# Optimization experiments

Measured on AMD Instinct MI355X. Metric: run time of the kernel, lower is better.

Reference implementation:

```python
import jax, jax.numpy as jnp
import numpy as np

N, L, V, D, E, NL = 50000, 32, 5000, 128, 800000, 3
P, B = 5000, 64

def setup_inputs() -> dict:
    key = jax.random.key(0)
    ks = jax.random.split(key, 6)
    x = jax.random.randint(ks[0], (N, L), 0, V)            # token ids, 0 = pad
    edge_index = jax.random.randint(ks[1], (2, E), 0, N)   # [2,E] src,dst
    pool_idx = jnp.arange(N) // (N // P)                   # node -> pooled supernode
    node_batch = pool_idx * B // P                         # node -> graph id (grouped, as in torch loop)
    embed = jax.random.normal(ks[2], (V, D), jnp.float32) * 0.02
    W_l = jax.random.normal(ks[3], (NL, D, D), jnp.float32) / np.sqrt(D)
    W_r = jax.random.normal(ks[4], (NL, D, D), jnp.float32) / np.sqrt(D)
    b = jnp.zeros((NL, D), jnp.float32)
    return dict(x=x, edge_index=edge_index, pool_idx=pool_idx, node_batch=node_batch,
                num_pooled=P, embed=embed, W_l=W_l, W_r=W_r, b=b)

def reference(x, edge_index, pool_idx, node_batch, num_pooled, embed, W_l, W_r, b):
    n = x.shape[0]
    dt = embed.dtype
    # masked mean-pool of token embeddings (pad id = 0), length clamped to >=1
    mask = (x != 0)
    lengths = jnp.clip(mask.sum(axis=1), 1, None).astype(dt)          # [N]
    h = (embed[x] * mask[..., None].astype(dt)).sum(axis=1) / lengths[:, None]  # [N,D]
    src, dst = edge_index[0], edge_index[1]
    deg = jnp.clip(jax.ops.segment_sum(jnp.ones(src.shape[0], dt), dst, num_segments=n), 1.0, None)
    # SAGEConv layers: mean-aggregate neighbors, lin_l(agg)+bias + lin_r(self), relu
    # (dropout p=0.5 is identity in eval mode)
    for i in range(W_l.shape[0]):
        agg = jax.ops.segment_sum(h[src], dst, num_segments=n) / deg[:, None]
        h = jax.nn.relu(agg @ W_l[i] + b[i] + h @ W_r[i])
    # global mean pool over supernodes
    cnt = jnp.clip(jax.ops.segment_sum(jnp.ones(n, dt), pool_idx, num_segments=num_pooled), 1.0, None)
    x_pooled = jax.ops.segment_sum(h, pool_idx, num_segments=num_pooled) / cnt[:, None]
    # global max pool of graph ids -> pooled batch vector
    batch_pooled = jax.ops.segment_max(node_batch, pool_idx, num_segments=num_pooled)
    # coalesced pooled edges without self-loops, as a dense boolean adjacency
    sp, dp = pool_idx[src], pool_idx[dst]
    adj = jnp.zeros((num_pooled, num_pooled), jnp.bool_).at[sp, dp].set(True)
    adj = adj & ~jnp.eye(num_pooled, dtype=jnp.bool_)
    return x_pooled, adj, batch_pooled
```

## Files before the change

kernel.cpp:

```cpp
#include <hip/hip_runtime.h>
#include <hip/hip_fp16.h>
#include <limits.h>

#define D 128
#define NBK 768
#define EB  2048
#define SCL 64.0f

typedef __attribute__((ext_vector_type(8))) short bf16x8;
typedef __attribute__((ext_vector_type(4))) float f32x4;
typedef __attribute__((ext_vector_type(2))) float f32x2;

#if __has_builtin(__builtin_amdgcn_cvt_pk_f32_fp8) && __has_builtin(__builtin_amdgcn_cvt_pk_fp8_f32)
#define HW_FP8 1
#endif

static __device__ __forceinline__ unsigned short f2bf(float f) {
    unsigned u = __builtin_bit_cast(unsigned, f);
    u += 0x7FFFu + ((u >> 16) & 1u);
    return (unsigned short)(u >> 16);
}
static __device__ __forceinline__ float bf2f(unsigned u16) {
    unsigned u = u16 << 16;
    return __builtin_bit_cast(float, u);
}
static __device__ __forceinline__ bf16x8 load_frag(const unsigned short* p) {
    uint4 v = *(const uint4*)p;
    return __builtin_bit_cast(bf16x8, v);
}
static __device__ __forceinline__ ushort4 pack4(const float* a, float s) {
    ushort4 o;
    o.x = f2bf(a[0] * s); o.y = f2bf(a[1] * s);
    o.z = f2bf(a[2] * s); o.w = f2bf(a[3] * s);
    return o;
}

static __device__ __forceinline__ unsigned char f2q(float v) {
#ifdef HW_FP8
    return (unsigned char)(__builtin_amdgcn_cvt_pk_fp8_f32(v, v, 0, false) & 0xff);
#else
    unsigned short u = __half_as_ushort(__float2half(v));
    u = (unsigned short)(u + 0x7F + ((u >> 8) & 1));
    return (unsigned char)(u >> 8);
#endif
}
static __device__ __forceinline__ unsigned enc4(float a0, float a1, float a2, float a3) {
#ifdef HW_FP8
    unsigned u = __builtin_amdgcn_cvt_pk_fp8_f32(a0, a1, 0, false);
    u = __builtin_amdgcn_cvt_pk_fp8_f32(a2, a3, (int)u, true);
    return u;
#else
    return (unsigned)f2q(a0) | ((unsigned)f2q(a1) << 8) |
           ((unsigned)f2q(a2) << 16) | ((unsigned)f2q(a3) << 24);
#endif
}
static __device__ __forceinline__ void dec4(float* a, unsigned u) {
#ifdef HW_FP8
    f32x2 lo = __builtin_amdgcn_cvt_pk_f32_fp8((int)u, false);
    f32x2 hi = __builtin_amdgcn_cvt_pk_f32_fp8((int)u, true);
    a[0] += lo.x; a[1] += lo.y; a[2] += hi.x; a[3] += hi.y;
#else
    a[0] += __half2float(__ushort_as_half((unsigned short)((u & 0xff) << 8)));
    a[1] += __half2float(__ushort_as_half((unsigned short)(((u >> 8) & 0xff) << 8)));
    a[2] += __half2float(__ushort_as_half((unsigned short)(((u >> 16) & 0xff) << 8)));
    a[3] += __half2float(__ushort_as_half((unsigned short)((u >> 24) << 8)));
#endif
}
static __device__ __forceinline__ void dec16(float* a, uint4 v) {
    dec4(a, v.x); dec4(a + 4, v.y); dec4(a + 8, v.z); dec4(a + 12, v.w);
}

__global__ __launch_bounds__(256) void zero_k(float4* __restrict__ b, size_t nb)
{
    size_t i = (size_t)blockIdx.x * 256 + threadIdx.x;
    if (i < nb) b[i] = make_float4(0.f, 0.f, 0.f, 0.f);
}

__global__ __launch_bounds__(256) void epack_k(
    const float* __restrict__ embed, unsigned* __restrict__ e8, int n4)
{
    int i = blockIdx.x * 256 + threadIdx.x;
    if (i >= n4) return;
    float4 v = *(const float4*)&embed[(size_t)i * 4];
    e8[i] = enc4(v.x * SCL, v.y * SCL, v.z * SCL, v.w * SCL);
}

__global__ __launch_bounds__(256) void embed_pool_k(
    const int* __restrict__ x, const unsigned char* __restrict__ e8,
    unsigned short* __restrict__ h16, unsigned char* __restrict__ h8, int n, int L)
{
    __shared__ int toks[16][32];
    int t = threadIdx.x;
    int sub = t >> 4, s = t & 15;
    int node = blockIdx.x * 16 + sub;
    for (int j = t; j < 16 * L; j += 256) {
        int nd = blockIdx.x * 16 + j / L;
        toks[j / L][j % L] = (nd < n) ? x[(size_t)nd * L + (j % L)] : 0;
    }
    __syncthreads();
    if (node >= n) return;
    float acc[8] = {};
    int cnt = 0;
    for (int l = 0; l < L; ++l) {
        int tok = toks[sub][l];
        if (tok != 0) {
            uint2 v = *(const uint2*)&e8[(size_t)tok * D + s * 8];
            dec4(acc, v.x); dec4(acc + 4, v.y);
            cnt++;
        }
    }
    float c = (float)(cnt > 0 ? cnt : 1);
    float invh = 1.0f / (SCL * c);
    float inv8 = 1.0f / c;
    ushort4 lo = pack4(acc, invh), hi = pack4(acc + 4, invh);
    *(ushort4*)&h16[(size_t)node * D + s * 8]     = lo;
    *(ushort4*)&h16[(size_t)node * D + s * 8 + 4] = hi;
    uint2 q;
    q.x = enc4(acc[0] * inv8, acc[1] * inv8, acc[2] * inv8, acc[3] * inv8);
    q.y = enc4(acc[4] * inv8, acc[5] * inv8, acc[6] * inv8, acc[7] * inv8);
    *(uint2*)&h8[(size_t)node * D + s * 8] = q;
}

__global__ __launch_bounds__(256) void wpack_k(
    const float* __restrict__ Wl, const float* __restrict__ Wr,
    unsigned short* __restrict__ Wp, int NL)
{
    int idx = blockIdx.x * 256 + threadIdx.x;
    if (idx >= NL * 2 * 16384) return;
    int m = idx >> 14;
    int r = idx & 16383;
    int j = r & 7;
    int lane = (r >> 3) & 63;
    int cb = (r >> 9) & 7;
    int kb = (r >> 12) & 3;
    const float* W = ((m & 1) ? Wr : Wl) + (size_t)(m >> 1) * D * D;
    int k = kb * 32 + (lane >> 4) * 8 + j;
    int c = cb * 16 + (lane & 15);
    Wp[idx] = f2bf(W[(size_t)k * D + c]);
}

__global__ __launch_bounds__(256) void deghist_k(
    const int* __restrict__ ei, const int* __restrict__ pool,
    int* __restrict__ degall, int E, int n, int P, int nblk)
{
    __shared__ int hist[NBK];
    int t = threadIdx.x;
    for (int i = t; i < NBK; i += 256) hist[i] = 0;
    __syncthreads();
    int base = blockIdx.x * EB;
    int lim = min(E, base + EB);
    for (int e = base + t; e < lim; e += 256) {
        int src = ei[e], dst = ei[E + e];
        atomicAdd(&degall[dst], 1);
        int sp = pool[src], dp = pool[dst];
        if (sp != dp) atomicAdd(&hist[(sp * P + dp) >> 15], 1);
    }
    __syncthreads();
    for (int i = t; i < NBK; i += 256)
        degall[n + i * nblk + blockIdx.x] = hist[i];
}

__global__ __launch_bounds__(256) void scan_partial_k(
    const int* __restrict__ deg, int* __restrict__ bsum, int n)
{
    int b = blockIdx.x, t = threadIdx.x;
    int i0 = b * 1024 + t * 4;
    int s = 0;
    #pragma unroll
    for (int k = 0; k < 4; ++k) { int i = i0 + k; if (i < n) s += deg[i]; }
    for (int off = 32; off > 0; off >>= 1) s += __shfl_down(s, off, 64);
    __shared__ int sm4[4];
    if ((t & 63) == 0) sm4[t >> 6] = s;
    __syncthreads();
    if (t == 0) bsum[b] = sm4[0] + sm4[1] + sm4[2] + sm4[3];
}

__global__ __launch_bounds__(512) void scan_bsum_k(
    const int* __restrict__ bsum, int* __restrict__ boff, int nb)
{
    __shared__ int sm[512];
    int t = threadIdx.x;
    sm[t] = (t < nb) ? bsum[t] : 0;
    __syncthreads();
    for (int off = 1; off < 512; off <<= 1) {
        int add = (t >= off) ? sm[t - off] : 0;
        __syncthreads();
        sm[t] += add;
        __syncthreads();
    }
    if (t < nb) boff[t] = (t > 0) ? sm[t - 1] : 0;
}

__global__ __launch_bounds__(256) void scan_final_k(
    const int* __restrict__ deg, const int* __restrict__ boff,
    int* __restrict__ rp, int n)
{
    __shared__ int sm[256];
    int b = blockIdx.x, t = threadIdx.x;
    int i0 = b * 1024 + t * 4;
    int v[4];
    #pragma unroll
    for (int k = 0; k < 4; ++k) { int i = i0 + k; v[k] = (i < n) ? deg[i] : 0; }
    v[1] += v[0]; v[2] += v[1]; v[3] += v[2];
    sm[t] = v[3];
    __syncthreads();
    for (int off = 1; off < 256; off <<= 1) {
        int add = (t >= off) ? sm[t - off] : 0;
        __syncthreads();
        sm[t] += add;
        __syncthreads();
    }
    int base = boff[b] + ((t > 0) ? sm[t - 1] : 0);
    if (b == 0 && t == 0) rp[0] = 0;
    #pragma unroll
    for (int k = 0; k < 4; ++k) {
        int i = i0 + k;
        if (i < n) rp[i + 1] = base + v[k];
    }
}

__global__ __launch_bounds__(256) void csr_scatter_k(
    const int* __restrict__ ei, const int* __restrict__ rpall,
    int* __restrict__ cur, int* __restrict__ col, int E)
{
    int e = blockIdx.x * 256 + threadIdx.x;
    if (e >= E) return;
    int src = ei[e], dst = ei[E + e];
    int pos = atomicAdd(&cur[dst], 1);
    col[rpall[dst] + pos] = src;
}

__global__ __launch_bounds__(256) void bkt_scatter_k(
    const int* __restrict__ ei, const int* __restrict__ rpall,
    const int* __restrict__ pool, int* __restrict__ kbuf,
    int E, int n, int P, int nblk)
{
    __shared__ int off[NBK];
    int t = threadIdx.x;
    for (int i = t; i < NBK; i += 256)
        off[i] = rpall[n + i * nblk + blockIdx.x] - E;
    __syncthreads();
    int base = blockIdx.x * EB;
    int lim = min(E, base + EB);
    for (int e = base + t; e < lim; e += 256) {
        int src = ei[e], dst = ei[E + e];
        int sp = pool[src], dp = pool[dst];
        if (sp != dp) {
            int key = sp * P + dp;
            int kpos = atomicAdd(&off[key >> 15], 1);
            kbuf[kpos] = key;
        }
    }
}

__global__ __launch_bounds__(256) void adj_write_k(
    const int* __restrict__ rpall, const int* __restrict__ kbuf,
    float* __restrict__ adj, int E, int n, int nblk, int ns)
{
    int b = blockIdx.x;
    int s = rpall[n + b * nblk] - E;
    int e = (b == NBK - 1) ? (rpall[ns] - E) : (rpall[n + (b + 1) * nblk] - E);
    for (int i = s + threadIdx.x; i < e; i += 256)
        adj[(size_t)kbuf[i]] = 1.0f;
}

__global__ __launch_bounds__(256) void aggregate_k(
    const unsigned char* __restrict__ h8, const int* __restrict__ rp,
    const int* __restrict__ col, unsigned short* __restrict__ agg16, int n)
{
    int node = blockIdx.x * 4 + (threadIdx.x >> 6);
    int lane = threadIdx.x & 63;
    if (node >= n) return;
    int beg = rp[node], end = rp[node + 1];
    int oct = lane >> 3, s = lane & 7;
    float acc[16] = {};
    int e = beg + oct;
    for (; e + 8 < end; e += 16) {
        uint4 v0 = *(const uint4*)&h8[(size_t)col[e] * D + s * 16];
        uint4 v1 = *(const uint4*)&h8[(size_t)col[e + 8] * D + s * 16];
        dec16(acc, v0);
        dec16(acc, v1);
    }
    if (e < end)
        dec16(acc, *(const uint4*)&h8[(size_t)col[e] * D + s * 16]);
    #pragma unroll
    for (int k = 0; k < 16; ++k) {
        acc[k] += __shfl_xor(acc[k], 8, 64);
        acc[k] += __shfl_xor(acc[k], 16, 64);
        acc[k] += __shfl_xor(acc[k], 32, 64);
    }
    if (oct == 0) {
        int dg = end - beg;
        float inv = 1.0f / (SCL * (float)(dg > 0 ? dg : 1));
        ushort4 o0 = pack4(acc, inv),     o1 = pack4(acc + 4, inv);
        ushort4 o2 = pack4(acc + 8, inv), o3 = pack4(acc + 12, inv);
        *(ushort4*)&agg16[(size_t)node * D + s * 16]      = o0;
        *(ushort4*)&agg16[(size_t)node * D + s * 16 + 4]  = o1;
        *(ushort4*)&agg16[(size_t)node * D + s * 16 + 8]  = o2;
        *(ushort4*)&agg16[(size_t)node * D + s * 16 + 12] = o3;
    }
}

__global__ __launch_bounds__(256) void sage_gemm_mfma_k(
    const unsigned short* __restrict__ agg16, unsigned short* __restrict__ h16,
    unsigned char* __restrict__ h8, const unsigned short* __restrict__ Wp,
    const float* __restrict__ bias, int n, int write8)
{
    int t = threadIdx.x;
    int w = t >> 6, lane = t & 63;
    int node0 = blockIdx.x * 128 + w * 32;
    int row = lane & 15, g = lane >> 4;

    f32x4 acc[2][8];
    #pragma unroll
    for (int i = 0; i < 2; ++i)
        #pragma unroll
        for (int c = 0; c < 8; ++c)
            acc[i][c] = (f32x4){0.f, 0.f, 0.f, 0.f};

    float bs[8];
    #pragma unroll
    for (int cb = 0; cb < 8; ++cb) bs[cb] = bias[cb * 16 + row];

    bool ok0 = (node0 < n);
    bool ok1 = (node0 + 16 < n);

    #pragma unroll
    for (int kb = 0; kb < 8; ++kb) {
        const unsigned short* Asrc = (kb < 4) ? agg16 : h16;
        int ko = (kb & 3) * 32 + g * 8;
        bf16x8 a0 = (bf16x8){0,0,0,0,0,0,0,0};
        bf16x8 a1 = a0;
        if (ok0) a0 = load_frag(&Asrc[(size_t)(node0 + row) * D + ko]);
        if (ok1) a1 = load_frag(&Asrc[(size_t)(node0 + 16 + row) * D + ko]);
        const unsigned short* wp = Wp + ((kb < 4) ? 0 : 16384) + (size_t)(kb & 3) * 4096;
        #pragma unroll
        for (int cb = 0; cb < 8; ++cb) {
            bf16x8 b = load_frag(&wp[(cb * 64 + lane) * 8]);
            acc[0][cb] = __builtin_amdgcn_mfma_f32_16x16x32_bf16(a0, b, acc[0][cb], 0, 0, 0);
            acc[1][cb] = __builtin_amdgcn_mfma_f32_16x16x32_bf16(a1, b, acc[1][cb], 0, 0, 0);
        }
    }

    #pragma unroll
    for (int rg = 0; rg < 2; ++rg) {
        int nb = node0 + rg * 16;
        if (nb >= n) break;
        #pragma unroll
        for (int cb = 0; cb < 8; ++cb) {
            int c = cb * 16 + row;
            #pragma unroll
            for (int j = 0; j < 4; ++j) {
                int node = nb + g * 4 + j;
                float v = fmaxf(acc[rg][cb][j] + bs[cb], 0.f);
                h16[(size_t)node * D + c] = f2bf(v);
                if (write8) h8[(size_t)node * D + c] = f2q(v * SCL);
            }
        }
    }
}

__global__ __launch_bounds__(128) void poolmean_k(
    const unsigned short* __restrict__ h16, const int* __restrict__ pool,
    const int* __restrict__ nbatch, float* __restrict__ outx,
    float* __restrict__ outb, int n, int P)
{
    int p = blockIdx.x;
    int d = threadIdx.x;
    int lo = 0, hi = n;
    while (lo < hi) { int mid = (lo + hi) >> 1; if (pool[mid] < p) lo = mid + 1; else hi = mid; }
    int s = lo;
    hi = n;
    while (lo < hi) { int mid = (lo + hi) >> 1; if (pool[mid] < p + 1) lo = mid + 1; else hi = mid; }
    int e = lo;
    float sum = 0.f;
    for (int i = s; i < e; ++i) sum += bf2f(h16[(size_t)i * D + d]);
    int c = e - s;
    outx[(size_t)p * D + d] = sum / (float)(c > 0 ? c : 1);
    if (d == 0) {
        int bm = INT_MIN;
        for (int i = s; i < e; ++i) bm = max(bm, nbatch[i]);
        outb[p] = (float)bm;
    }
}

extern "C" void kernel_launch(void* const* d_in, const int* in_sizes, int n_in,
                              void* d_out, int out_size, void* d_ws, size_t ws_size,
                              hipStream_t stream)
{
    const int*   x      = (const int*)d_in[0];
    const int*   ei     = (const int*)d_in[1];
    const int*   pool   = (const int*)d_in[2];
    const int*   nbatch = (const int*)d_in[3];
    const float* embed  = (const float*)d_in[5];
    const float* Wl     = (const float*)d_in[6];
    const float* Wr     = (const float*)d_in[7];
    const float* bias   = (const float*)d_in[8];

    const int N  = in_sizes[2];
    const int L  = in_sizes[0] / N;
    const int E  = in_sizes[1] / 2;
    const int VD = in_sizes[5];
    const int NL = in_sizes[6] / (D * D);
    const int P  = 5000;

    float* out_x   = (float*)d_out;
    float* out_adj = out_x + (size_t)P * D;
    float* out_b   = out_adj + (size_t)P * P;

    char* w = (char*)d_ws;
    auto alloc = [&](size_t bytes) { void* p = w; w += (bytes + 255) & ~255ULL; return p; };
    size_t ND = (size_t)N * D;
    unsigned short* h16   = (unsigned short*)alloc(ND * 2);
    unsigned short* agg16 = (unsigned short*)alloc(ND * 2);
    unsigned char*  h8    = (unsigned char*)alloc(ND);
    unsigned short* Wp    = (unsigned short*)alloc((size_t)NL * 2 * 16384 * 2);
    unsigned char*  e8    = (unsigned char*)alloc((size_t)VD);

    const int NBLK = (E + EB - 1) / EB;
    const int NS   = N + NBK * NBLK;
    const int NB   = (NS + 1023) / 1024;

    int*   col    = (int*)alloc((size_t)E * 4);
    int*   kbuf   = (int*)alloc((size_t)E * 4);
    int*   rpall  = (int*)alloc((size_t)(NS + 1) * 4);
    int*   bsum   = (int*)alloc(512 * 4);
    int*   boff   = (int*)alloc(512 * 4);
    int*   degall = (int*)alloc((size_t)(NS + N) * 4);
    int*   cur    = degall + NS;

    size_t nz = ((size_t)(NS + N) + 3) / 4;
    zero_k<<<(int)((nz + 255) / 256), 256, 0, stream>>>((float4*)degall, nz);

    epack_k<<<(VD / 4 + 255) / 256, 256, 0, stream>>>(embed, (unsigned*)e8, VD / 4);
    wpack_k<<<(NL * 2 * 16384 + 255) / 256, 256, 0, stream>>>(Wl, Wr, Wp, NL);
    embed_pool_k<<<(N + 15) / 16, 256, 0, stream>>>(x, e8, h16, h8, N, L);
    deghist_k<<<NBLK, 256, 0, stream>>>(ei, pool, degall, E, N, P, NBLK);
    scan_partial_k<<<NB, 256, 0, stream>>>(degall, bsum, NS);
    scan_bsum_k<<<1, 512, 0, stream>>>(bsum, boff, NB);
    scan_final_k<<<NB, 256, 0, stream>>>(degall, boff, rpall, NS);
    csr_scatter_k<<<(E + 255) / 256, 256, 0, stream>>>(ei, rpall, cur, col, E);
    bkt_scatter_k<<<NBLK, 256, 0, stream>>>(ei, rpall, pool, kbuf, E, N, P, NBLK);
    adj_write_k<<<NBK, 256, 0, stream>>>(rpall, kbuf, out_adj, E, N, NBLK, NS);

    for (int ly = 0; ly < NL; ++ly) {
        aggregate_k<<<(N + 3) / 4, 256, 0, stream>>>(h8, rpall, col, agg16, N);
        sage_gemm_mfma_k<<<(N + 127) / 128, 256, 0, stream>>>(
            agg16, h16, h8, Wp + (size_t)ly * 2 * 16384, bias + (size_t)ly * D, N,
            (ly < NL - 1) ? 1 : 0);
    }

    poolmean_k<<<P, 128, 0, stream>>>(h16, pool, nbatch, out_x, out_b, N, P);
}
```

Baseline: 308.9 us.

## Replace bucketed adjacency scatter with atomic bitmap and dense expand

The pooled adjacency is now built by setting bits in a P*P bitmap with atomicOr, then one kernel expands every bitmap word into 32 float writes covering the whole dense output. This drops the per-block histogram, the extended scan over the bucket counts, the key scatter and the sparse adjacency write, so the scan now covers only node degrees. The trade is that every element of the 25M-float adjacency is written by the expand kernel, and the bitmap is zeroed in the same launch as the degree arrays. The aggregate kernel is also reworked to use 16 lanes with 8-byte loads per edge (4 edges in flight instead of 8), and the pool-mean loop is unrolled into four accumulators.

```diff
diff --git a/kernel.cpp b/kernel.cpp
--- a/kernel.cpp
+++ b/kernel.cpp
@@ -3,8 +3,6 @@
 #include <limits.h>
 
 #define D 128
-#define NBK 768
-#define EB  2048
 #define SCL 64.0f
 
 typedef __attribute__((ext_vector_type(8))) short bf16x8;
@@ -66,14 +64,14 @@
     a[3] += __half2float(__ushort_as_half((unsigned short)((u >> 24) << 8)));
 #endif
 }
-static __device__ __forceinline__ void dec16(float* a, uint4 v) {
-    dec4(a, v.x); dec4(a + 4, v.y); dec4(a + 8, v.z); dec4(a + 12, v.w);
-}
-
-__global__ __launch_bounds__(256) void zero_k(float4* __restrict__ b, size_t nb)
+
+__global__ __launch_bounds__(256) void zero_k(
+    float4* __restrict__ a, size_t na, float4* __restrict__ b, size_t nb)
 {
     size_t i = (size_t)blockIdx.x * 256 + threadIdx.x;
-    if (i < nb) b[i] = make_float4(0.f, 0.f, 0.f, 0.f);
+    float4 z = make_float4(0.f, 0.f, 0.f, 0.f);
+    if (i < na) a[i] = z;
+    else if (i - na < nb) b[i - na] = z;
 }
 
 __global__ __launch_bounds__(256) void epack_k(
@@ -83,42 +81,6 @@
     if (i >= n4) return;
     float4 v = *(const float4*)&embed[(size_t)i * 4];
     e8[i] = enc4(v.x * SCL, v.y * SCL, v.z * SCL, v.w * SCL);
-}
-
-__global__ __launch_bounds__(256) void embed_pool_k(
-    const int* __restrict__ x, const unsigned char* __restrict__ e8,
-    unsigned short* __restrict__ h16, unsigned char* __restrict__ h8, int n, int L)
-{
-    __shared__ int toks[16][32];
-    int t = threadIdx.x;
-    int sub = t >> 4, s = t & 15;
-    int node = blockIdx.x * 16 + sub;
-    for (int j = t; j < 16 * L; j += 256) {
-        int nd = blockIdx.x * 16 + j / L;
-        toks[j / L][j % L] = (nd < n) ? x[(size_t)nd * L + (j % L)] : 0;
-    }
-    __syncthreads();
-    if (node >= n) return;
-    float acc[8] = {};
-    int cnt = 0;
-    for (int l = 0; l < L; ++l) {
-        int tok = toks[sub][l];
-        if (tok != 0) {
-            uint2 v = *(const uint2*)&e8[(size_t)tok * D + s * 8];
-            dec4(acc, v.x); dec4(acc + 4, v.y);
-            cnt++;
-        }
-    }
-    float c = (float)(cnt > 0 ? cnt : 1);
-    float invh = 1.0f / (SCL * c);
-    float inv8 = 1.0f / c;
-    ushort4 lo = pack4(acc, invh), hi = pack4(acc + 4, invh);
-    *(ushort4*)&h16[(size_t)node * D + s * 8]     = lo;
-    *(ushort4*)&h16[(size_t)node * D + s * 8 + 4] = hi;
-    uint2 q;
-    q.x = enc4(acc[0] * inv8, acc[1] * inv8, acc[2] * inv8, acc[3] * inv8);
-    q.y = enc4(acc[4] * inv8, acc[5] * inv8, acc[6] * inv8, acc[7] * inv8);
-    *(uint2*)&h8[(size_t)node * D + s * 8] = q;
 }
 
 __global__ __launch_bounds__(256) void wpack_k(
@@ -139,25 +101,55 @@
     Wp[idx] = f2bf(W[(size_t)k * D + c]);
 }
 
-__global__ __launch_bounds__(256) void deghist_k(
+__global__ __launch_bounds__(256) void embed_pool_k(
+    const int* __restrict__ x, const unsigned char* __restrict__ e8,
+    unsigned short* __restrict__ h16, unsigned char* __restrict__ h8, int n, int L)
+{
+    __shared__ int toks[16][32];
+    int t = threadIdx.x;
+    int sub = t >> 4, s = t & 15;
+    int node = blockIdx.x * 16 + sub;
+    for (int j = t; j < 16 * L; j += 256) {
+        int nd = blockIdx.x * 16 + j / L;
+        toks[j / L][j % L] = (nd < n) ? x[(size_t)nd * L + (j % L)] : 0;
+    }
+    __syncthreads();
+    if (node >= n) return;
+    float acc[8] = {};
+    int cnt = 0;
+    for (int l = 0; l < L; ++l) {
+        int tok = toks[sub][l];
+        if (tok != 0) {
+            uint2 v = *(const uint2*)&e8[(size_t)tok * D + s * 8];
+            dec4(acc, v.x); dec4(acc + 4, v.y);
+            cnt++;
+        }
+    }
+    float c = (float)(cnt > 0 ? cnt : 1);
+    float invh = 1.0f / (SCL * c);
+    float inv8 = 1.0f / c;
+    ushort4 lo = pack4(acc, invh), hi = pack4(acc + 4, invh);
+    *(ushort4*)&h16[(size_t)node * D + s * 8]     = lo;
+    *(ushort4*)&h16[(size_t)node * D + s * 8 + 4] = hi;
+    uint2 q;
+    q.x = enc4(acc[0] * inv8, acc[1] * inv8, acc[2] * inv8, acc[3] * inv8);
+    q.y = enc4(acc[4] * inv8, acc[5] * inv8, acc[6] * inv8, acc[7] * inv8);
+    *(uint2*)&h8[(size_t)node * D + s * 8] = q;
+}
+
+__global__ __launch_bounds__(256) void deg_adj_k(
     const int* __restrict__ ei, const int* __restrict__ pool,
-    int* __restrict__ degall, int E, int n, int P, int nblk)
-{
-    __shared__ int hist[NBK];
-    int t = threadIdx.x;
-    for (int i = t; i < NBK; i += 256) hist[i] = 0;
-    __syncthreads();
-    int base = blockIdx.x * EB;
-    int lim = min(E, base + EB);
-    for (int e = base + t; e < lim; e += 256) {
-        int src = ei[e], dst = ei[E + e];
-        atomicAdd(&degall[dst], 1);
-        int sp = pool[src], dp = pool[dst];
-        if (sp != dp) atomicAdd(&hist[(sp * P + dp) >> 15], 1);
-    }
-    __syncthreads();
-    for (int i = t; i < NBK; i += 256)
-        degall[n + i * nblk + blockIdx.x] = hist[i];
+    int* __restrict__ deg, unsigned* __restrict__ bitmap, int E, int P)
+{
+    int e = blockIdx.x * 256 + threadIdx.x;
+    if (e >= E) return;
+    int src = ei[e], dst = ei[E + e];
+    atomicAdd(&deg[dst], 1);
+    int sp = pool[src], dp = pool[dst];
+    if (sp != dp) {
+        unsigned key = (unsigned)(sp * P + dp);
+        atomicOr(&bitmap[key >> 5], 1u << (key & 31));
+    }
 }
 
 __global__ __launch_bounds__(256) void scan_partial_k(
@@ -175,14 +167,14 @@
     if (t == 0) bsum[b] = sm4[0] + sm4[1] + sm4[2] + sm4[3];
 }
 
-__global__ __launch_bounds__(512) void scan_bsum_k(
+__global__ __launch_bounds__(256) void scan_bsum_k(
     const int* __restrict__ bsum, int* __restrict__ boff, int nb)
 {
-    __shared__ int sm[512];
+    __shared__ int sm[256];
     int t = threadIdx.x;
     sm[t] = (t < nb) ? bsum[t] : 0;
     __syncthreads();
-    for (int off = 1; off < 512; off <<= 1) {
+    for (int off = 1; off < 256; off <<= 1) {
         int add = (t >= off) ? sm[t - off] : 0;
         __syncthreads();
         sm[t] += add;
@@ -220,48 +212,33 @@
 }
 
 __global__ __launch_bounds__(256) void csr_scatter_k(
-    const int* __restrict__ ei, const int* __restrict__ rpall,
+    const int* __restrict__ ei, const int* __restrict__ rp,
     int* __restrict__ cur, int* __restrict__ col, int E)
 {
     int e = blockIdx.x * 256 + threadIdx.x;
     if (e >= E) return;
     int src = ei[e], dst = ei[E + e];
     int pos = atomicAdd(&cur[dst], 1);
-    col[rpall[dst] + pos] = src;
-}
-
-__global__ __launch_bounds__(256) void bkt_scatter_k(
-    const int* __restrict__ ei, const int* __restrict__ rpall,
-    const int* __restrict__ pool, int* __restrict__ kbuf,
-    int E, int n, int P, int nblk)
-{
-    __shared__ int off[NBK];
-    int t = threadIdx.x;
-    for (int i = t; i < NBK; i += 256)
-        off[i] = rpall[n + i * nblk + blockIdx.x] - E;
-    __syncthreads();
-    int base = blockIdx.x * EB;
-    int lim = min(E, base + EB);
-    for (int e = base + t; e < lim; e += 256) {
-        int src = ei[e], dst = ei[E + e];
-        int sp = pool[src], dp = pool[dst];
-        if (sp != dp) {
-            int key = sp * P + dp;
-            int kpos = atomicAdd(&off[key >> 15], 1);
-            kbuf[kpos] = key;
-        }
-    }
-}
-
-__global__ __launch_bounds__(256) void adj_write_k(
-    const int* __restrict__ rpall, const int* __restrict__ kbuf,
-    float* __restrict__ adj, int E, int n, int nblk, int ns)
-{
-    int b = blockIdx.x;
-    int s = rpall[n + b * nblk] - E;
-    int e = (b == NBK - 1) ? (rpall[ns] - E) : (rpall[n + (b + 1) * nblk] - E);
-    for (int i = s + threadIdx.x; i < e; i += 256)
-        adj[(size_t)kbuf[i]] = 1.0f;
+    col[rp[dst] + pos] = src;
+}
+
+__global__ __launch_bounds__(256) void adj_expand_k(
+    const unsigned* __restrict__ bitmap, float* __restrict__ adj, int nw)
+{
+    int i = blockIdx.x * 256 + threadIdx.x;
+    if (i >= nw) return;
+    unsigned b = bitmap[i];
+    float4 v[8];
+    #pragma unroll
+    for (int k = 0; k < 8; ++k) {
+        v[k].x = (b >> (4 * k + 0)) & 1 ? 1.0f : 0.0f;
+        v[k].y = (b >> (4 * k + 1)) & 1 ? 1.0f : 0.0f;
+        v[k].z = (b >> (4 * k + 2)) & 1 ? 1.0f : 0.0f;
+        v[k].w = (b >> (4 * k + 3)) & 1 ? 1.0f : 0.0f;
+    }
+    float4* dst = (float4*)(adj + (size_t)i * 32);
+    #pragma unroll
+    for (int k = 0; k < 8; ++k) dst[k] = v[k];
 }
 
 __global__ __launch_bounds__(256) void aggregate_k(
@@ -272,32 +249,31 @@
     int lane = threadIdx.x & 63;
     if (node >= n) return;
     int beg = rp[node], end = rp[node + 1];
-    int oct = lane >> 3, s = lane & 7;
-    float acc[16] = {};
-    int e = beg + oct;
-    for (; e + 8 < end; e += 16) {
-        uint4 v0 = *(const uint4*)&h8[(size_t)col[e] * D + s * 16];
-        uint4 v1 = *(const uint4*)&h8[(size_t)col[e + 8] * D + s * 16];
-        dec16(acc, v0);
-        dec16(acc, v1);
-    }
-    if (e < end)
-        dec16(acc, *(const uint4*)&h8[(size_t)col[e] * D + s * 16]);
-    #pragma unroll
-    for (int k = 0; k < 16; ++k) {
-        acc[k] += __shfl_xor(acc[k], 8, 64);
+    int q = lane >> 4, s = lane & 15;
+    float acc[8] = {};
+    int e = beg + q;
+    for (; e + 4 < end; e += 8) {
+        int c0 = col[e], c1 = col[e + 4];
+        uint2 v0 = *(const uint2*)&h8[(size_t)c0 * D + s * 8];
+        uint2 v1 = *(const uint2*)&h8[(size_t)c1 * D + s * 8];
+        dec4(acc, v0.x); dec4(acc + 4, v0.y);
+        dec4(acc, v1.x); dec4(acc + 4, v1.y);
+    }
+    if (e < end) {
+        uint2 v0 = *(const uint2*)&h8[(size_t)col[e] * D + s * 8];
+        dec4(acc, v0.x); dec4(acc + 4, v0.y);
+    }
+    #pragma unroll
+    for (int k = 0; k < 8; ++k) {
         acc[k] += __shfl_xor(acc[k], 16, 64);
         acc[k] += __shfl_xor(acc[k], 32, 64);
     }
-    if (oct == 0) {
+    if (q == 0) {
         int dg = end - beg;
         float inv = 1.0f / (SCL * (float)(dg > 0 ? dg : 1));
-        ushort4 o0 = pack4(acc, inv),     o1 = pack4(acc + 4, inv);
-        ushort4 o2 = pack4(acc + 8, inv), o3 = pack4(acc + 12, inv);
-        *(ushort4*)&agg16[(size_t)node * D + s * 16]      = o0;
-        *(ushort4*)&agg16[(size_t)node * D + s * 16 + 4]  = o1;
-        *(ushort4*)&agg16[(size_t)node * D + s * 16 + 8]  = o2;
-        *(ushort4*)&agg16[(size_t)node * D + s * 16 + 12] = o3;
+        ushort4 lo = pack4(acc, inv), hi = pack4(acc + 4, inv);
+        *(ushort4*)&agg16[(size_t)node * D + s * 8]     = lo;
+        *(ushort4*)&agg16[(size_t)node * D + s * 8 + 4] = hi;
     }
 }
 
@@ -373,13 +349,21 @@
     hi = n;
     while (lo < hi) { int mid = (lo + hi) >> 1; if (pool[mid] < p + 1) lo = mid + 1; else hi = mid; }
     int e = lo;
-    float sum = 0.f;
-    for (int i = s; i < e; ++i) sum += bf2f(h16[(size_t)i * D + d]);
+    float s0 = 0.f, s1 = 0.f, s2 = 0.f, s3 = 0.f;
+    int i = s;
+    for (; i + 3 < e; i += 4) {
+        s0 += bf2f(h16[(size_t)(i + 0) * D + d]);
+        s1 += bf2f(h16[(size_t)(i + 1) * D + d]);
+        s2 += bf2f(h16[(size_t)(i + 2) * D + d]);
+        s3 += bf2f(h16[(size_t)(i + 3) * D + d]);
+    }
+    for (; i < e; ++i) s0 += bf2f(h16[(size_t)i * D + d]);
+    float sum = (s0 + s1) + (s2 + s3);
     int c = e - s;
     outx[(size_t)p * D + d] = sum / (float)(c > 0 ? c : 1);
     if (d == 0) {
         int bm = INT_MIN;
-        for (int i = s; i < e; ++i) bm = max(bm, nbatch[i]);
+        for (int j = s; j < e; ++j) bm = max(bm, nbatch[j]);
         outb[p] = (float)bm;
     }
 }
@@ -416,35 +400,34 @@
     unsigned char*  h8    = (unsigned char*)alloc(ND);
     unsigned short* Wp    = (unsigned short*)alloc((size_t)NL * 2 * 16384 * 2);
     unsigned char*  e8    = (unsigned char*)alloc((size_t)VD);
-
-    const int NBLK = (E + EB - 1) / EB;
-    const int NS   = N + NBK * NBLK;
-    const int NB   = (NS + 1023) / 1024;
-
     int*   col    = (int*)alloc((size_t)E * 4);
-    int*   kbuf   = (int*)alloc((size_t)E * 4);
-    int*   rpall  = (int*)alloc((size_t)(NS + 1) * 4);
-    int*   bsum   = (int*)alloc(512 * 4);
-    int*   boff   = (int*)alloc(512 * 4);
-    int*   degall = (int*)alloc((size_t)(NS + N) * 4);
-    int*   cur    = degall + NS;
-
-    size_t nz = ((size_t)(NS + N) + 3) / 4;
-    zero_k<<<(int)((nz + 255) / 256), 256, 0, stream>>>((float4*)degall, nz);
+    int*   rp     = (int*)alloc((size_t)(N + 1) * 4);
+    int*   bsum   = (int*)alloc(256 * 4);
+    int*   boff   = (int*)alloc(256 * 4);
+    const int NW  = (P * P + 31) / 32;
+    int*      deg    = (int*)alloc((size_t)N * 2 * 4);
+    int*      cur    = deg + N;
+    unsigned* bitmap = (unsigned*)alloc(((size_t)NW + 4) * 4);
+
+    const int NB = (N + 1023) / 1024;
+
+    size_t na = ((size_t)N * 2 + 3) / 4;
+    size_t nbm = ((size_t)NW + 3) / 4;
+    zero_k<<<(int)((na + nbm + 255) / 256), 256, 0, stream>>>(
+        (float4*)deg, na, (float4*)bitmap, nbm);
 
     epack_k<<<(VD / 4 + 255) / 256, 256, 0, stream>>>(embed, (unsigned*)e8, VD / 4);
     wpack_k<<<(NL * 2 * 16384 + 255) / 256, 256, 0, stream>>>(Wl, Wr, Wp, NL);
     embed_pool_k<<<(N + 15) / 16, 256, 0, stream>>>(x, e8, h16, h8, N, L);
-    deghist_k<<<NBLK, 256, 0, stream>>>(ei, pool, degall, E, N, P, NBLK);
-    scan_partial_k<<<NB, 256, 0, stream>>>(degall, bsum, NS);
-    scan_bsum_k<<<1, 512, 0, stream>>>(bsum, boff, NB);
-    scan_final_k<<<NB, 256, 0, stream>>>(degall, boff, rpall, NS);
-    csr_scatter_k<<<(E + 255) / 256, 256, 0, stream>>>(ei, rpall, cur, col, E);
-    bkt_scatter_k<<<NBLK, 256, 0, stream>>>(ei, rpall, pool, kbuf, E, N, P, NBLK);
-    adj_write_k<<<NBK, 256, 0, stream>>>(rpall, kbuf, out_adj, E, N, NBLK, NS);
+    deg_adj_k<<<(E + 255) / 256, 256, 0, stream>>>(ei, pool, deg, bitmap, E, P);
+    scan_partial_k<<<NB, 256, 0, stream>>>(deg, bsum, N);
+    scan_bsum_k<<<1, 256, 0, stream>>>(bsum, boff, NB);
+    scan_final_k<<<NB, 256, 0, stream>>>(deg, boff, rp, N);
+    csr_scatter_k<<<(E + 255) / 256, 256, 0, stream>>>(ei, rp, cur, col, E);
+    adj_expand_k<<<(NW + 255) / 256, 256, 0, stream>>>(bitmap, out_adj, NW);
 
     for (int ly = 0; ly < NL; ++ly) {
-        aggregate_k<<<(N + 3) / 4, 256, 0, stream>>>(h8, rpall, col, agg16, N);
+        aggregate_k<<<(N + 3) / 4, 256, 0, stream>>>(h8, rp, col, agg16, N);
         sage_gemm_mfma_k<<<(N + 127) / 128, 256, 0, stream>>>(
             agg16, h16, h8, Wp + (size_t)ly * 2 * 16384, bias + (size_t)ly * D, N,
             (ly < NL - 1) ? 1 : 0);
```

After: 333.1 us. 1.08x slower.
